# Kernel tuning notes

Measured on AMD Instinct MI355X. Metric: run time of the kernel, lower is better.

The kernel has to match this reference:

```python
import jax, jax.numpy as jnp
import numpy as np

B, T, NT = 2, 2048, 512
DIM, DEPTH, MEL, TDIM = 768, 8, 100, 512
D_INNER, NS, PH, Q = 1536, 128, 64, 64
NH = D_INNER // PH
CONV_DIM = D_INNER + 2 * NS
D_INPROJ = 2 * D_INNER + 2 * NS + NH
KCONV = 4
FFI = 2 * DIM
VOCAB = 257


def _ln(x, eps=1e-6):
    m = jnp.mean(x, -1, keepdims=True)
    v = jnp.mean((x - m) ** 2, -1, keepdims=True)
    return (x - m) * jax.lax.rsqrt(v + eps)


def _mish(x):
    return x * jnp.tanh(jax.nn.softplus(x))


def _dwconv_causal(x, w, b):
    # x: [B,T,C], w: [C,K]  depthwise causal conv (left-pad K-1)
    K = w.shape[1]
    xp = jnp.pad(x, ((0, 0), (K - 1, 0), (0, 0)))
    y = sum(xp[:, k:k + x.shape[1]] * w[:, k] for k in range(K))
    return y + b


def _ssd(xh, Bm, Cm, dt, A):
    # chunked selective-scan (Mamba SSD form). xh [B,T,H,P]; Bm,Cm [B,T,N]; dt [B,T,H]; A [H]
    Bsz, Tt, H, P = xh.shape
    N = Bm.shape[-1]
    Cn = Tt // Q
    xb = (dt[..., None] * xh).reshape(Bsz, Cn, Q, H, P)
    a = (dt * A).reshape(Bsz, Cn, Q, H)
    Bc = Bm.reshape(Bsz, Cn, Q, N)
    Cc = Cm.reshape(Bsz, Cn, Q, N)
    acum = jnp.cumsum(a, axis=2)  # [b,c,q,h]
    # intra-chunk: decay matrix exp(acum_q - acum_s) for s <= q
    Ldec = jnp.exp(acum[:, :, :, None, :] - acum[:, :, None, :, :])  # [b,c,q,s,h]
    mask = jnp.tril(jnp.ones((Q, Q), dtype=bool))
    Ldec = jnp.where(mask[None, None, :, :, None], Ldec, 0.0)
    CB = jnp.einsum('bcqn,bcsn->bcqs', Cc, Bc)
    y_in = jnp.einsum('bcqs,bcqsh,bcshp->bcqhp', CB, Ldec, xb)
    # chunk end-states
    dst = jnp.exp(acum[:, :, -1:, :] - acum)  # [b,c,q,h]
    S = jnp.einsum('bcqh,bcqn,bcqhp->bchpn', dst, Bc, xb)
    atot = jnp.exp(acum[:, :, -1, :])  # [b,c,h] total chunk decay

    def step(Hc, inp):
        at_c, S_c = inp
        return at_c[:, :, None, None] * Hc + S_c, Hc

    H0 = jnp.zeros((Bsz, H, P, N), xh.dtype)
    _, prev = jax.lax.scan(step, H0, (jnp.moveaxis(atot, 1, 0), jnp.moveaxis(S, 1, 0)))
    prev = jnp.moveaxis(prev, 0, 1)  # state entering each chunk [b,c,h,p,n]
    y_out = jnp.einsum('bcqn,bchpn->bcqhp', Cc, prev) * jnp.exp(acum)[..., None]
    return (y_in + y_out).reshape(Bsz, Tt, H, P)


def _forward(x, cond, time, text, text_table, inp_w, inp_b, pos_w1, pos_b1, pos_w2, pos_b2, t_w1, t_b1, t_w2, t_b2, adaln_w, adaln_b, in_w, conv_w, conv_b, dt_bias, A_log, Dp, rms_w, out_w, ff_w1, ff_b1, ff_w2, ff_b2, fin_w, fin_b, proj_w, proj_b):
    # timestep embedding (sinusoidal, scale 1000, freq dim 256 -> MLP)
    half = 128
    freqs = jnp.exp(-jnp.log(10000.0) / (half - 1) * jnp.arange(half, dtype=x.dtype))
    ang = 1000.0 * time[:, None] * freqs[None]
    te = jnp.concatenate([jnp.sin(ang), jnp.cos(ang)], -1)
    tvec = jax.nn.silu(te @ t_w1 + t_b1) @ t_w2 + t_b2  # [B,DIM]
    # text embedding (conv_layers=0 path): shift by 1, pad to seq_len, lookup
    idx = jnp.pad(text + 1, ((0, 0), (0, T - text.shape[1])))
    temb = text_table[idx]  # [B,T,TDIM]
    # input embedding + ConvPositionEmbedding (grouped conv k=31, groups=16, Mish x2)
    h = jnp.concatenate([x, cond, temb], -1) @ inp_w + inp_b  # [B,T,DIM]
    dn = ('NWC', 'WIO', 'NWC')
    p = jax.lax.conv_general_dilated(h, pos_w1, (1,), [(15, 15)], dimension_numbers=dn, feature_group_count=16) + pos_b1
    p = _mish(p)
    p = jax.lax.conv_general_dilated(p, pos_w2, (1,), [(15, 15)], dimension_numbers=dn, feature_group_count=16) + pos_b2
    h = h + _mish(p)
    st = jax.nn.silu(tvec)
    for l in range(DEPTH):
        mod = st @ adaln_w[l] + adaln_b[l]
        sh_msa, sc_msa, g_msa, sh_mlp, sc_mlp, g_mlp = jnp.split(mod, 6, -1)
        xn = _ln(h) * (1 + sc_msa[:, None]) + sh_msa[:, None]
        # Mamba-3 selective scan block
        zxbcdt = xn @ in_w[l]
        z = zxbcdt[..., :D_INNER]
        xBC = zxbcdt[..., D_INNER:D_INNER + CONV_DIM]
        dt = zxbcdt[..., D_INNER + CONV_DIM:]
        xBC = jax.nn.silu(_dwconv_causal(xBC, conv_w[l], conv_b[l]))
        xp = xBC[..., :D_INNER].reshape(B, T, NH, PH)
        Bm = xBC[..., D_INNER:D_INNER + NS]
        Cm = xBC[..., D_INNER + NS:]
        dt = jax.nn.softplus(dt + dt_bias[l])
        A = -jnp.exp(A_log[l])
        y = _ssd(xp, Bm, Cm, dt, A) + Dp[l][:, None] * xp
        y = y.reshape(B, T, D_INNER) * jax.nn.silu(z)
        y = y * jax.lax.rsqrt(jnp.mean(y * y, -1, keepdims=True) + 1e-5) * rms_w[l]
        h = h + g_msa[:, None] * (y @ out_w[l])
        # gated FFN
        xn = _ln(h) * (1 + sc_mlp[:, None]) + sh_mlp[:, None]
        ff = jax.nn.gelu(xn @ ff_w1[l] + ff_b1[l], approximate=True) @ ff_w2[l] + ff_b2[l]
        h = h + g_mlp[:, None] * ff
    fm = st @ fin_w + fin_b
    sc, sh = jnp.split(fm, 2, -1)
    h = _ln(h) * (1 + sc[:, None]) + sh[:, None]
    return h @ proj_w + proj_b


def setup_inputs() -> dict:
    key = jax.random.key(0)
    it = iter(jax.random.split(key, 40))

    def n(shape, s=0.02):
        return (s * jax.random.normal(next(it), shape)).astype(jnp.float32)

    inp = {
        'x': n((B, T, MEL), 1.0),
        'cond': n((B, T, MEL), 1.0),
        'time': jax.random.uniform(next(it), (B,), dtype=jnp.float32),
        'text_table': n((VOCAB, TDIM)),
        'inp_w': n((2 * MEL + TDIM, DIM)), 'inp_b': jnp.zeros((DIM,), jnp.float32),
        'pos_w1': n((31, DIM // 16, DIM), 0.05), 'pos_b1': jnp.zeros((DIM,), jnp.float32),
        'pos_w2': n((31, DIM // 16, DIM), 0.05), 'pos_b2': jnp.zeros((DIM,), jnp.float32),
        't_w1': n((256, DIM)), 't_b1': jnp.zeros((DIM,), jnp.float32),
        't_w2': n((DIM, DIM)), 't_b2': jnp.zeros((DIM,), jnp.float32),
        'adaln_w': n((DEPTH, DIM, 6 * DIM)), 'adaln_b': jnp.zeros((DEPTH, 6 * DIM), jnp.float32),
        'in_w': n((DEPTH, DIM, D_INPROJ)),
        'conv_w': n((DEPTH, CONV_DIM, KCONV), 0.2), 'conv_b': jnp.zeros((DEPTH, CONV_DIM), jnp.float32),
        'dt_bias': n((DEPTH, NH), 0.5),
        'A_log': jnp.log(jnp.tile(jnp.arange(1, NH + 1, dtype=jnp.float32), (DEPTH, 1))),
        'Dp': jnp.ones((DEPTH, NH), jnp.float32),
        'rms_w': jnp.ones((DEPTH, D_INNER), jnp.float32),
        'out_w': n((DEPTH, D_INNER, DIM)),
        'ff_w1': n((DEPTH, DIM, FFI)), 'ff_b1': jnp.zeros((DEPTH, FFI), jnp.float32),
        'ff_w2': n((DEPTH, FFI, DIM)), 'ff_b2': jnp.zeros((DEPTH, DIM), jnp.float32),
        'fin_w': n((DIM, 2 * DIM)), 'fin_b': jnp.zeros((2 * DIM,), jnp.float32),
        'proj_w': n((DIM, MEL)), 'proj_b': jnp.zeros((MEL,), jnp.float32),
    }
    inp['text'] = jax.random.randint(next(it), (B, NT), 0, 256)
    return inp


def reference(x, cond, time, text, text_table, inp_w, inp_b, pos_w1, pos_b1, pos_w2, pos_b2, t_w1, t_b1, t_w2, t_b2, adaln_w, adaln_b, in_w, conv_w, conv_b, dt_bias, A_log, Dp, rms_w, out_w, ff_w1, ff_b1, ff_w2, ff_b2, fin_w, fin_b, proj_w, proj_b):
    return _forward(x, cond, time, text, text_table, inp_w, inp_b, pos_w1, pos_b1, pos_w2, pos_b2, t_w1, t_b1, t_w2, t_b2, adaln_w, adaln_b, in_w, conv_w, conv_b, dt_bias, A_log, Dp, rms_w, out_w, ff_w1, ff_b1, ff_w2, ff_b2, fin_w, fin_b, proj_w, proj_b)
```

## Files before the change

### kernel.cpp

```cpp
#include <hip/hip_runtime.h>
#include <math.h>

constexpr int Bv = 2, Tv = 2048, NTv = 512;
constexpr int DIMv = 768, DEPTHv = 8, MELv = 100, TDIMv = 512;
constexpr int DINNER = 1536, NSv = 128, PHv = 64, QQv = 64;
constexpr int NHv = DINNER / PHv;
constexpr int CONVD = DINNER + 2 * NSv;
constexpr int DINP = 2 * DINNER + 2 * NSv + NHv;
constexpr int KCONVv = 4, FFIv = 2 * DIMv;
constexpr int CNv = Tv / QQv;
constexpr int PCK = 1504;
constexpr int KCAT = 768;

typedef unsigned short u16;
typedef unsigned int u32;
typedef __attribute__((ext_vector_type(8))) short short8v;
typedef __attribute__((ext_vector_type(4))) float f32x4;

__device__ __forceinline__ float siluf(float x) { return x / (1.f + expf(-x)); }
__device__ __forceinline__ float softplusf(float x) { return x > 20.f ? x : log1pf(expf(x)); }
__device__ __forceinline__ float mishf(float x) { return x * tanhf(softplusf(x)); }

__device__ __forceinline__ u16 f2bf(float v) {
    u32 u = __builtin_bit_cast(u32, v);
    u32 r = (u + 0x7fffu + ((u >> 16) & 1u)) >> 16;
    return (u16)r;
}
__device__ __forceinline__ float bf2f(u16 v) {
    u32 u = (u32)v << 16;
    return __builtin_bit_cast(float, u);
}
__device__ __forceinline__ float bf2fs(short v) { return bf2f((u16)v); }

__device__ __forceinline__ void gload16(const void* g, void* l) {
    __builtin_amdgcn_global_load_lds(
        (const __attribute__((address_space(1))) u32*)g,
        (__attribute__((address_space(3))) u32*)l, 16, 0, 0);
}

__device__ __forceinline__ float blockReduceSum(float v) {
    __shared__ float red[4];
    #pragma unroll
    for (int off = 32; off > 0; off >>= 1) v += __shfl_down(v, off, 64);
    __syncthreads();
    if ((threadIdx.x & 63) == 0) red[threadIdx.x >> 6] = v;
    __syncthreads();
    return red[0] + red[1] + red[2] + red[3];
}

template <int EPI>
__device__ __forceinline__ void gemm_epi(f32x4* acc, int nfrag, int row, int col,
        int N, int ldc, const float* bias, float* Cf, u16* Cb,
        const float* modv, int goff, int mstride) {
    if (col >= N) return;
    const float bv = (EPI == 1 || EPI == 2 || EPI == 4) ? bias[col] : 0.f;
    #pragma unroll
    for (int r = 0; r < 4; r++) {
        float v = (*acc)[r] + bv;
        if (EPI == 0) {
            Cb[(size_t)(row + r) * ldc + col] = f2bf(v);
        } else if (EPI == 2) {
            float xx = v;
            v = 0.5f * xx * (1.f + tanhf(0.7978845608028654f * (xx + 0.044715f * xx * xx * xx)));
            Cb[(size_t)(row + r) * ldc + col] = f2bf(v);
        } else if (EPI == 3 || EPI == 4) {
            const int bb = (row + r) >> 11;
            float g = modv[(size_t)bb * mstride + goff + col];
            Cf[(size_t)(row + r) * ldc + col] += g * v;
        } else {
            Cf[(size_t)(row + r) * ldc + col] = v;
        }
    }
}

template <int EPI>
__global__ __launch_bounds__(256) void gemm_bf16(const u16* __restrict__ A,
        const u16* __restrict__ BT, const float* __restrict__ bias,
        float* __restrict__ Cf, u16* __restrict__ Cb,
        int M, int N, int K, int ldc,
        const float* __restrict__ modv, int goff, int mstride) {
    __shared__ __align__(16) u16 As[2][128 * 32];
    __shared__ __align__(16) u16 Bs[2][128 * 32];
    const int tid = threadIdx.x;
    const int gx = gridDim.x;
    const int nwg = gx * gridDim.y;
    int flat = blockIdx.y * gx + blockIdx.x;
    const int qq = nwg >> 3;
    flat = (flat & 7) * qq + (flat >> 3);
    const int m0 = (flat / gx) * 128, n0 = (flat % gx) * 128;
    const int lane = tid & 63;
    const int wid = tid >> 6;
    const int wm = (wid >> 1) * 64, wn = (wid & 1) * 64;
    f32x4 acc[4][4] = {};
    const int srow = tid >> 2, sseg = (tid & 3) * 8;
    const u16* Ag = A + (size_t)(m0 + srow) * K + sseg;
    const u16* Bg = BT + (size_t)(n0 + srow) * K + sseg;
    const int lr = lane & 15, lk = (lane >> 4) * 8;
    gload16(Ag, &As[0][tid * 8]);
    gload16(Ag + (size_t)64 * K, &As[0][tid * 8 + 64 * 32]);
    gload16(Bg, &Bs[0][tid * 8]);
    gload16(Bg + (size_t)64 * K, &Bs[0][tid * 8 + 64 * 32]);
    __syncthreads();
    int cur = 0;
    for (int k0 = 0; k0 < K; k0 += 32) {
        if (k0 + 32 < K) {
            const int nb = cur ^ 1, kn = k0 + 32;
            gload16(Ag + kn, &As[nb][tid * 8]);
            gload16(Ag + kn + (size_t)64 * K, &As[nb][tid * 8 + 64 * 32]);
            gload16(Bg + kn, &Bs[nb][tid * 8]);
            gload16(Bg + kn + (size_t)64 * K, &Bs[nb][tid * 8 + 64 * 32]);
        }
        short8v a_f[4], b_f[4];
        #pragma unroll
        for (int i = 0; i < 4; i++)
            a_f[i] = *(const short8v*)&As[cur][(wm + i * 16 + lr) * 32 + lk];
        #pragma unroll
        for (int j = 0; j < 4; j++)
            b_f[j] = *(const short8v*)&Bs[cur][(wn + j * 16 + lr) * 32 + lk];
        #pragma unroll
        for (int i = 0; i < 4; i++)
            #pragma unroll
            for (int j = 0; j < 4; j++)
                acc[i][j] = __builtin_amdgcn_mfma_f32_16x16x32_bf16(a_f[i], b_f[j], acc[i][j], 0, 0, 0);
        __syncthreads();
        cur ^= 1;
    }
    const int r0 = (lane >> 4) * 4;
    #pragma unroll
    for (int i = 0; i < 4; i++)
        #pragma unroll
        for (int j = 0; j < 4; j++)
            gemm_epi<EPI>(&acc[i][j], 1, m0 + wm + i * 16 + r0, n0 + wn + j * 16 + lr,
                          N, ldc, bias, Cf, Cb, modv, goff, mstride);
}

template <int EPI>
__global__ __launch_bounds__(256) void gemm_bf16s(const u16* __restrict__ A,
        const u16* __restrict__ BT, const float* __restrict__ bias,
        float* __restrict__ Cf, u16* __restrict__ Cb,
        int M, int N, int K, int ldc,
        const float* __restrict__ modv, int goff, int mstride) {
    __shared__ __align__(16) u16 As[4][64 * 32];
    __shared__ __align__(16) u16 Bs[4][128 * 32];
    const int tid = threadIdx.x;
    const int gx = gridDim.x;
    const int nwg = gx * gridDim.y;
    int flat = blockIdx.y * gx + blockIdx.x;
    const int qq = nwg >> 3;
    flat = (flat & 7) * qq + (flat >> 3);
    const int m0 = (flat / gx) * 64, n0 = (flat % gx) * 128;
    const int lane = tid & 63;
    const int wid = tid >> 6;
    const int wn = wid * 32;
    f32x4 acc[4][2] = {};
    const int srow = tid >> 2, sseg = (tid & 3) * 8;
    const u16* Ag = A + (size_t)(m0 + srow) * K + sseg;
    const u16* Bg = BT + (size_t)(n0 + srow) * K + sseg;
    const int lr = lane & 15, lk = (lane >> 4) * 8;
    auto STAGE = [&](int buf, int kk) {
        gload16(Ag + kk, &As[buf][tid * 8]);
        gload16(Bg + kk, &Bs[buf][tid * 8]);
        gload16(Bg + kk + (size_t)64 * K, &Bs[buf][tid * 8 + 64 * 32]);
    };
    auto COMP = [&](int buf) {
        short8v a_f[4], b_f[2];
        #pragma unroll
        for (int i = 0; i < 4; i++)
            a_f[i] = *(const short8v*)&As[buf][(i * 16 + lr) * 32 + lk];
        #pragma unroll
        for (int j = 0; j < 2; j++)
            b_f[j] = *(const short8v*)&Bs[buf][(wn + j * 16 + lr) * 32 + lk];
        #pragma unroll
        for (int i = 0; i < 4; i++)
            #pragma unroll
            for (int j = 0; j < 2; j++)
                acc[i][j] = __builtin_amdgcn_mfma_f32_16x16x32_bf16(a_f[i], b_f[j], acc[i][j], 0, 0, 0);
    };
    STAGE(0, 0);
    STAGE(1, 32);
    __syncthreads();
    int cur = 0;
    for (int k0 = 0; k0 < K; k0 += 64) {
        if (k0 + 64 < K) {
            STAGE((cur + 2) & 3, k0 + 64);
            STAGE((cur + 3) & 3, k0 + 96);
        }
        COMP(cur);
        COMP((cur + 1) & 3);
        __syncthreads();
        cur = (cur + 2) & 3;
    }
    const int r0 = (lane >> 4) * 4;
    #pragma unroll
    for (int i = 0; i < 4; i++)
        #pragma unroll
        for (int j = 0; j < 2; j++)
            gemm_epi<EPI>(&acc[i][j], 1, m0 + i * 16 + r0, n0 + wn + j * 16 + lr,
                          N, ldc, bias, Cf, Cb, modv, goff, mstride);
}

__global__ __launch_bounds__(256) void wt_convert_b(const float* __restrict__ W,
        u16* __restrict__ WT, int Kd, int N, int Kmax, int Npad) {
    const float* Wl = W + (size_t)blockIdx.z * Kmax * N;
    u16* WTl = WT + (size_t)blockIdx.z * Npad * Kd;
    __shared__ float t[32][33];
    const int n0 = blockIdx.x * 32, k0 = blockIdx.y * 32;
    const int c = threadIdx.x & 31, rq = (threadIdx.x >> 5) * 4;
    #pragma unroll
    for (int i = 0; i < 4; i++) {
        int n = n0 + c, k = k0 + rq + i;
        t[rq + i][c] = (n < N && k < Kmax) ? Wl[(size_t)k * N + n] : 0.f;
    }
    __syncthreads();
    #pragma unroll
    for (int i = 0; i < 4; i++)
        WTl[(size_t)(n0 + rq + i) * Kd + k0 + c] = f2bf(t[c][rq + i]);
}

__global__ __launch_bounds__(256) void pw_convert(const float* __restrict__ w,
        u16* __restrict__ WT) {
    __shared__ float t[32][33];
    const int kk0 = blockIdx.x * 32, o0 = blockIdx.y * 32;
    const int c = threadIdx.x & 31, rq = (threadIdx.x >> 5) * 4;
    #pragma unroll
    for (int i = 0; i < 4; i++) {
        int kk = kk0 + rq + i;
        t[rq + i][c] = (kk < 1488) ? w[(size_t)kk * DIMv + o0 + c] : 0.f;
    }
    __syncthreads();
    #pragma unroll
    for (int i = 0; i < 4; i++)
        WT[(size_t)(o0 + rq + i) * PCK + kk0 + c] = f2bf(t[c][rq + i]);
}

template <int IN_BF, int FUSE>
__global__ __launch_bounds__(256) void posconv_mfma(const void* __restrict__ inv,
        const u16* __restrict__ WT, const float* __restrict__ bias,
        void* __restrict__ outv) {
    __shared__ __align__(16) u16 xs[95 * 48];
    const int t0 = blockIdx.x * 64, g = blockIdx.y, b = blockIdx.z;
    const int tid = threadIdx.x;
    for (int e = tid; e < 95 * 48; e += 256) {
        int rr = e / 48, cc = e % 48;
        int t = t0 - 15 + rr;
        float v = 0.f;
        if (t >= 0 && t < Tv) {
            size_t gi = ((size_t)b * Tv + t) * DIMv + g * 48 + cc;
            v = IN_BF ? bf2f(((const u16*)inv)[gi]) : ((const float*)inv)[gi];
        }
        xs[e] = f2bf(v);
    }
    __syncthreads();
    const int lane = tid & 63, w = tid >> 6;
    const int lr = lane & 15, lq8 = (lane >> 4) * 8, rq = (lane >> 4) * 4;
    const u16* arow = &xs[(w * 16 + lr) * 48 + lq8];
    const u16* brow = &WT[(size_t)(g * 48 + lr) * PCK + lq8];
    f32x4 acc[3] = {};
    #pragma unroll 2
    for (int ks = 0; ks < PCK / 32; ks++) {
        short8v a = *(const short8v*)(arow + ks * 32);
        #pragma unroll
        for (int j = 0; j < 3; j++) {
            short8v bf = *(const short8v*)(brow + (size_t)j * 16 * PCK + ks * 32);
            acc[j] = __builtin_amdgcn_mfma_f32_16x16x32_bf16(a, bf, acc[j], 0, 0, 0);
        }
    }
    #pragma unroll
    for (int j = 0; j < 3; j++) {
        const int o = g * 48 + j * 16 + lr;
        const float bvv = bias[o];
        #pragma unroll
        for (int r = 0; r < 4; r++) {
            const int t = t0 + w * 16 + rq + r;
            float v = acc[j][r] + bvv;
            size_t gi = ((size_t)b * Tv + t) * DIMv + o;
            if (FUSE == 0) ((u16*)outv)[gi] = f2bf(mishf(v));
            else ((float*)outv)[gi] += mishf(v);
        }
    }
}

__global__ __launch_bounds__(256) void temb1_kernel(const float* __restrict__ timev,
        const float* __restrict__ t_w1, const float* __restrict__ t_b1,
        float* __restrict__ hid) {
    const int b = blockIdx.y;
    const int o = blockIdx.x * 64 + (threadIdx.x & 63);
    const int ks = threadIdx.x >> 6;
    __shared__ float te[256];
    __shared__ float part[4][64];
    {
        int j = threadIdx.x, f = j & 127;
        float fr = expf(-logf(10000.f) / 127.f * (float)f);
        float ang = 1000.f * timev[b] * fr;
        te[j] = (j < 128) ? sinf(ang) : cosf(ang);
    }
    __syncthreads();
    float acc = 0.f;
    #pragma unroll 8
    for (int k = ks * 64; k < ks * 64 + 64; k++) acc += te[k] * t_w1[(size_t)k * DIMv + o];
    part[ks][threadIdx.x & 63] = acc;
    __syncthreads();
    if (threadIdx.x < 64) {
        float r = part[0][threadIdx.x] + part[1][threadIdx.x] + part[2][threadIdx.x] + part[3][threadIdx.x]
                + t_b1[o];
        hid[b * DIMv + o] = siluf(r);
    }
}

__global__ __launch_bounds__(256) void temb2_kernel(const float* __restrict__ hid,
        const float* __restrict__ t_w2, const float* __restrict__ t_b2,
        float* __restrict__ st_out) {
    const int b = blockIdx.y;
    const int o = blockIdx.x * 64 + (threadIdx.x & 63);
    const int ks = threadIdx.x >> 6;
    __shared__ float hv[DIMv];
    __shared__ float part[4][64];
    for (int j = threadIdx.x; j < DIMv; j += 256) hv[j] = hid[b * DIMv + j];
    __syncthreads();
    float acc = 0.f;
    #pragma unroll 8
    for (int k = ks * 192; k < ks * 192 + 192; k++) acc += hv[k] * t_w2[(size_t)k * DIMv + o];
    part[ks][threadIdx.x & 63] = acc;
    __syncthreads();
    if (threadIdx.x < 64) {
        float r = part[0][threadIdx.x] + part[1][threadIdx.x] + part[2][threadIdx.x] + part[3][threadIdx.x]
                + t_b2[o];
        st_out[b * DIMv + o] = siluf(r);
    }
}

__global__ __launch_bounds__(256) void modvec_kernel(const float* __restrict__ st,
        const float* __restrict__ W, const float* __restrict__ bias,
        float* __restrict__ out, int N) {
    const int l = blockIdx.z, b = blockIdx.y;
    const int o = blockIdx.x * 64 + (threadIdx.x & 63);
    const int ks = threadIdx.x >> 6;
    __shared__ float sv[DIMv];
    __shared__ float part[4][64];
    for (int j = threadIdx.x; j < DIMv; j += 256) sv[j] = st[b * DIMv + j];
    __syncthreads();
    const float* Wl = W + (size_t)l * DIMv * N + o;
    float acc = 0.f;
    #pragma unroll 8
    for (int k = ks * 192; k < ks * 192 + 192; k++) acc += sv[k] * Wl[(size_t)k * N];
    part[ks][threadIdx.x & 63] = acc;
    __syncthreads();
    if (threadIdx.x < 64) {
        float r = part[0][threadIdx.x] + part[1][threadIdx.x] + part[2][threadIdx.x] + part[3][threadIdx.x]
                + bias[(size_t)l * N + o];
        out[((size_t)l * Bv + b) * N + o] = r;
    }
}

__global__ void concat_bf16(const float* __restrict__ x, const float* __restrict__ cond,
                            const float* __restrict__ table, const int* __restrict__ text,
                            u16* __restrict__ cat) {
    size_t i = (size_t)blockIdx.x * 256 + threadIdx.x;
    const size_t total = (size_t)Bv * Tv * KCAT;
    if (i >= total) return;
    int j = (int)(i % KCAT);
    size_t row = i / KCAT;
    int t = (int)(row % Tv), b = (int)(row / Tv);
    float v = 0.f;
    if (j < MELv) v = x[row * MELv + j];
    else if (j < 2 * MELv) v = cond[row * MELv + (j - MELv)];
    else if (j < 712) {
        int idx = (t < NTv) ? (text[b * NTv + t] + 1) : 0;
        v = table[(size_t)idx * TDIMv + (j - 2 * MELv)];
    }
    cat[i] = f2bf(v);
}

template <int BF>
__global__ __launch_bounds__(256) void ln_mod_kernel(const float* __restrict__ h,
        void* __restrict__ outv, const float* __restrict__ modv,
        int sc_off, int sh_off, int mod_stride) {
    const int row = blockIdx.x;
    const int b = row / Tv;
    const float* hr = h + (size_t)row * DIMv;
    float s = 0.f;
    for (int j = threadIdx.x; j < DIMv; j += 256) s += hr[j];
    s = blockReduceSum(s);
    const float m = s / DIMv;
    float v = 0.f;
    for (int j = threadIdx.x; j < DIMv; j += 256) { float d = hr[j] - m; v += d * d; }
    v = blockReduceSum(v);
    const float rstd = rsqrtf(v / DIMv + 1e-6f);
    const float* mb = modv + (size_t)b * mod_stride;
    for (int j = threadIdx.x; j < DIMv; j += 256) {
        float val = (hr[j] - m) * rstd * (1.f + mb[sc_off + j]) + mb[sh_off + j];
        if (BF) ((u16*)outv)[(size_t)row * DIMv + j] = f2bf(val);
        else ((float*)outv)[(size_t)row * DIMv + j] = val;
    }
}

__global__ __launch_bounds__(256) void dwconvT(const u16* __restrict__ zxb,
        const float* __restrict__ cw, const float* __restrict__ cb,
        u16* __restrict__ xT) {
    __shared__ __align__(16) u16 in_s[67 * 72];
    const int pb = blockIdx.x;
    const int c = blockIdx.y, b = blockIdx.z;
    const int bc = b * CNv + c;
    const int tid = threadIdx.x;
    for (int e = tid; e < 67 * 8; e += 256) {
        int sp = e >> 3, p8 = (e & 7) * 8;
        int t = c * 64 + sp - 3;
        short8v v = {};
        if (t >= 0)
            v = *(const short8v*)&zxb[((size_t)b * Tv + t) * DINP + DINNER + pb * 64 + p8];
        *(short8v*)&in_s[sp * 72 + p8] = v;
    }
    __syncthreads();
    const int p = tid >> 2, sb = (tid & 3) * 16;
    const int ch = pb * 64 + p;
    const float w0 = cw[ch * 4], w1 = cw[ch * 4 + 1], w2 = cw[ch * 4 + 2], w3 = cw[ch * 4 + 3];
    const float bb = cb[ch];
    short8v o0, o1;
    #pragma unroll
    for (int i = 0; i < 16; i++) {
        int s = sb + i;
        float acc = bb + bf2f(in_s[s * 72 + p]) * w0 + bf2f(in_s[(s + 1) * 72 + p]) * w1
                  + bf2f(in_s[(s + 2) * 72 + p]) * w2 + bf2f(in_s[(s + 3) * 72 + p]) * w3;
        short r = (short)f2bf(siluf(acc));
        if (i < 8) o0[i] = r; else o1[i - 8] = r;
    }
    u16* dst = xT + ((size_t)bc * DINNER + ch) * 64 + sb;
    *(short8v*)dst = o0;
    *(short8v*)(dst + 8) = o1;
}

__global__ __launch_bounds__(256) void ssd_cb(const u16* __restrict__ zxb,
        const float* __restrict__ cw, const float* __restrict__ cbv,
        u16* __restrict__ xbcBC, float* __restrict__ CBg, u16* __restrict__ BTg) {
    constexpr int ST = 136;
    __shared__ __align__(16) u16 Cs[64 * ST];
    __shared__ __align__(16) u16 Bs[64 * ST];
    const int c = blockIdx.x, b = blockIdx.y;
    const int bc = b * CNv + c;
    const int tid = threadIdx.x;
    const size_t rowbase = (size_t)b * Tv + (size_t)c * QQv;
    for (int e = tid; e < 64 * 32; e += 256) {
        int r = e >> 5, n8 = (e & 31) * 8;
        size_t row = rowbase + r;
        int t = c * 64 + r;
        const u16* base = zxb + row * DINP + DINNER + n8;
        float acc[8];
        #pragma unroll
        for (int u = 0; u < 8; u++) acc[u] = cbv[DINNER + n8 + u];
        #pragma unroll
        for (int k = 0; k < KCONVv; k++) {
            const int d = k - 3;
            if (t + d < 0) continue;
            short8v tv = *(const short8v*)(base + (ptrdiff_t)d * DINP);
            #pragma unroll
            for (int u = 0; u < 8; u++)
                acc[u] += bf2fs(tv[u]) * cw[(DINNER + n8 + u) * KCONVv + k];
        }
        short8v o;
        #pragma unroll
        for (int u = 0; u < 8; u++) o[u] = (short)f2bf(siluf(acc[u]));
        if (n8 < NSv) *(short8v*)&Bs[r * ST + n8] = o;
        else *(short8v*)&Cs[r * ST + (n8 - NSv)] = o;
        *(short8v*)&xbcBC[row * 256 + n8] = o;
    }
    __syncthreads();
    u16* btg = BTg + (size_t)bc * (NSv * QQv);
    for (int e = tid; e < 128 * 64; e += 256) {
        int n = e >> 6, s = e & 63;
        btg[e] = Bs[s * ST + n];
    }
    const int lane = tid & 63, w = tid >> 6;
    const int lr = lane & 15, lk8 = (lane >> 4) * 8, rq = (lane >> 4) * 4;
    f32x4 acc[4] = {};
    #pragma unroll
    for (int ks = 0; ks < 4; ks++) {
        short8v a = *(const short8v*)&Cs[(w * 16 + lr) * ST + ks * 32 + lk8];
        #pragma unroll
        for (int j = 0; j < 4; j++) {
            short8v bf = *(const short8v*)&Bs[(j * 16 + lr) * ST + ks * 32 + lk8];
            acc[j] = __builtin_amdgcn_mfma_f32_16x16x32_bf16(a, bf, acc[j], 0, 0, 0);
        }
    }
    float* out = CBg + (size_t)bc * 4096;
    #pragma unroll
    for (int j = 0; j < 4; j++)
        #pragma unroll
        for (int r = 0; r < 4; r++)
            out[(w * 16 + rq + r) * 64 + j * 16 + lr] = acc[j][r];
}

__global__ __launch_bounds__(256) void ssd_part1m(const u16* __restrict__ xT,
        const u16* __restrict__ BTg, const u16* __restrict__ zxb,
        const float* __restrict__ dt_bias, const float* __restrict__ A_log,
        const float* __restrict__ CBg, u16* __restrict__ ybuf,
        u16* __restrict__ Sg, float* __restrict__ acg, float* __restrict__ atg) {
    constexpr int ST64 = 72;
    __shared__ __align__(16) u16 xTs[64 * ST64];
    __shared__ __align__(16) u16 Wsm[64 * ST64];
    __shared__ __align__(16) u16 BTs[128 * ST64];
    __shared__ float ac[64], dts[64], dtrev[64];
    const int h = blockIdx.x, c = blockIdx.y, b = blockIdx.z;
    const int bc = b * CNv + c;
    const int tid = threadIdx.x;
    const size_t rowbase = (size_t)b * Tv + (size_t)c * QQv;
    const size_t bch = ((size_t)bc) * NHv + h;
    if (tid < 64) {
        float raw = bf2f(zxb[(rowbase + tid) * DINP + DINNER + CONVD + h]) + dt_bias[h];
        float dtv = softplusf(raw);
        dts[tid] = dtv;
        float v = dtv * (-expf(A_log[h]));
        #pragma unroll
        for (int off = 1; off < 64; off <<= 1) {
            float t = __shfl_up(v, off, 64);
            if (tid >= off) v += t;
        }
        ac[tid] = v;
        float v63 = __shfl(v, 63, 64);
        dtrev[tid] = dtv * expf(v63 - v);
        acg[bch * 64 + tid] = v;
        if (tid == 63) atg[bch] = expf(v63);
    }
    {
        const u16* src = xT + ((size_t)bc * DINNER + h * PHv) * 64;
        for (int e = tid; e < 64 * 8; e += 256) {
            int p = e >> 3, s8 = (e & 7) * 8;
            *(short8v*)&xTs[p * ST64 + s8] = *(const short8v*)(src + p * 64 + s8);
        }
    }
    __syncthreads();
    {
        const u16* btg = BTg + (size_t)bc * (NSv * QQv);
        for (int e = tid; e < 128 * 8; e += 256) {
            int n = e >> 3, s8 = (e & 7) * 8;
            short8v v = *(const short8v*)(btg + n * 64 + s8);
            short8v o;
            #pragma unroll
            for (int u = 0; u < 8; u++)
                o[u] = (short)f2bf(bf2fs(v[u]) * dtrev[s8 + u]);
            *(short8v*)&BTs[n * ST64 + s8] = o;
        }
        const float* cbrow = CBg + (size_t)bc * 4096;
        for (int e = tid; e < 1024; e += 256) {
            int q = e >> 4, s4 = (e & 15) * 4;
            f32x4 cb4 = *(const f32x4*)&cbrow[q * 64 + s4];
            float aq = ac[q];
            #pragma unroll
            for (int u = 0; u < 4; u++) {
                int s = s4 + u;
                float wv = (s <= q) ? cb4[u] * expf(aq - ac[s]) * dts[s] : 0.f;
                Wsm[q * ST64 + s] = f2bf(wv);
            }
        }
    }
    __syncthreads();
    const int lane = tid & 63, w = tid >> 6;
    const int lr = lane & 15, lk8 = (lane >> 4) * 8, rq = (lane >> 4) * 4;
    {
        f32x4 acc[4] = {};
        #pragma unroll
        for (int ks = 0; ks < 2; ks++) {
            short8v bf = *(const short8v*)&xTs[(w * 16 + lr) * ST64 + ks * 32 + lk8];
            #pragma unroll
            for (int i = 0; i < 4; i++) {
                short8v a = *(const short8v*)&Wsm[(i * 16 + lr) * ST64 + ks * 32 + lk8];
                acc[i] = __builtin_amdgcn_mfma_f32_16x16x32_bf16(a, bf, acc[i], 0, 0, 0);
            }
        }
        #pragma unroll
        for (int i = 0; i < 4; i++)
            #pragma unroll
            for (int r = 0; r < 4; r++) {
                int q = i * 16 + rq + r, p = w * 16 + lr;
                ybuf[(rowbase + q) * DINNER + h * PHv + p] = f2bf(acc[i][r]);
            }
    }
    {
        f32x4 acc[4][2] = {};
        #pragma unroll
        for (int ks = 0; ks < 2; ks++) {
            short8v a[4];
            #pragma unroll
            for (int i = 0; i < 4; i++)
                a[i] = *(const short8v*)&xTs[(i * 16 + lr) * ST64 + ks * 32 + lk8];
            #pragma unroll
            for (int j = 0; j < 2; j++) {
                short8v bf = *(const short8v*)&BTs[(w * 32 + j * 16 + lr) * ST64 + ks * 32 + lk8];
                #pragma unroll
                for (int i = 0; i < 4; i++)
                    acc[i][j] = __builtin_amdgcn_mfma_f32_16x16x32_bf16(a[i], bf, acc[i][j], 0, 0, 0);
            }
        }
        u16* So = Sg + bch * (PHv * NSv);
        #pragma unroll
        for (int i = 0; i < 4; i++)
            #pragma unroll
            for (int j = 0; j < 2; j++)
                #pragma unroll
                for (int r = 0; r < 4; r++)
                    So[(i * 16 + rq + r) * NSv + w * 32 + j * 16 + lr] = f2bf(acc[i][j][r]);
    }
}

__global__ void ssd_scan(u16* __restrict__ Sg, const float* __restrict__ atg) {
    int idx = blockIdx.x * 256 + threadIdx.x;
    if (idx >= Bv * NHv * PHv * NSv) return;
    int n = idx % NSv;
    int p = (idx / NSv) % PHv;
    int h = (idx / (NSv * PHv)) % NHv;
    int b = idx / (NSv * PHv * NHv);
    float H = 0.f;
    for (int c = 0; c < CNv; c++) {
        size_t bch = ((size_t)b * CNv + c) * NHv + h;
        size_t off = bch * PHv * NSv + (size_t)p * NSv + n;
        float s = bf2f(Sg[off]);
        float at = atg[bch];
        Sg[off] = f2bf(H);
        H = at * H + s;
    }
}

__global__ __launch_bounds__(256) void ssd_part2m(const u16* __restrict__ xbcBC,
        const u16* __restrict__ xT, const u16* __restrict__ Sg,
        const float* __restrict__ acg, const float* __restrict__ Dp,
        u16* __restrict__ ybuf) {
    constexpr int ST = 136;
    __shared__ __align__(16) u16 Cs[64 * ST];
    __shared__ __align__(16) u16 Ps[64 * ST];
    __shared__ float eac[64];
    const int h = blockIdx.x, c = blockIdx.y, b = blockIdx.z;
    const int bc = b * CNv + c;
    const int tid = threadIdx.x;
    const size_t rowbase = (size_t)b * Tv + (size_t)c * QQv;
    const size_t bch = ((size_t)bc) * NHv + h;
    if (tid < 64) eac[tid] = expf(acg[bch * 64 + tid]);
    for (int e = tid; e < 64 * 16; e += 256) {
        int r = e >> 4, n8 = (e & 15) * 8;
        *(short8v*)&Cs[r * ST + n8] =
            *(const short8v*)&xbcBC[(rowbase + r) * 256 + NSv + n8];
        *(short8v*)&Ps[r * ST + n8] =
            *(const short8v*)&Sg[bch * (PHv * NSv) + (size_t)r * NSv + n8];
    }
    __syncthreads();
    const int lane = tid & 63, w = tid >> 6;
    const int lr = lane & 15, lk8 = (lane >> 4) * 8, rq = (lane >> 4) * 4;
    f32x4 acc[4] = {};
    #pragma unroll
    for (int ks = 0; ks < 4; ks++) {
        short8v bf = *(const short8v*)&Ps[(w * 16 + lr) * ST + ks * 32 + lk8];
        #pragma unroll
        for (int i = 0; i < 4; i++) {
            short8v a = *(const short8v*)&Cs[(i * 16 + lr) * ST + ks * 32 + lk8];
            acc[i] = __builtin_amdgcn_mfma_f32_16x16x32_bf16(a, bf, acc[i], 0, 0, 0);
        }
    }
    const float Dh = Dp[h];
    const int p = w * 16 + lr;
    const u16* xrow = xT + ((size_t)bc * DINNER + h * PHv + p) * 64;
    #pragma unroll
    for (int i = 0; i < 4; i++)
        #pragma unroll
        for (int r = 0; r < 4; r++) {
            int q = i * 16 + rq + r;
            size_t yi = (rowbase + q) * DINNER + h * PHv + p;
            float xv = bf2f(xrow[q]);
            ybuf[yi] = f2bf(bf2f(ybuf[yi]) + acc[i][r] * eac[q] + Dh * xv);
        }
}

__global__ __launch_bounds__(256) void gate_rms_kernel(const u16* __restrict__ y,
        const u16* __restrict__ zxb, const float* __restrict__ rms_w,
        u16* __restrict__ yb) {
    const int row = blockIdx.x;
    const u16* yr = y + (size_t)row * DINNER;
    const u16* zr = zxb + (size_t)row * DINP;
    float vals[8];
    float ss = 0.f;
    const int tid = threadIdx.x;
    if (tid < 192) {
        short8v yv = *(const short8v*)(yr + tid * 8);
        short8v zv = *(const short8v*)(zr + tid * 8);
        #pragma unroll
        for (int u = 0; u < 8; u++) {
            float v = bf2fs(yv[u]) * siluf(bf2fs(zv[u]));
            vals[u] = v;
            ss += v * v;
        }
    }
    ss = blockReduceSum(ss);
    const float scale = rsqrtf(ss / DINNER + 1e-5f);
    if (tid < 192) {
        short8v outv;
        #pragma unroll
        for (int u = 0; u < 8; u++)
            outv[u] = (short)f2bf(vals[u] * scale * rms_w[tid * 8 + u]);
        *(short8v*)(yb + (size_t)row * DINNER + tid * 8) = outv;
    }
}

extern "C" void kernel_launch(void* const* d_in, const int* in_sizes, int n_in,
                              void* d_out, int out_size, void* d_ws, size_t ws_size,
                              hipStream_t stream) {
    int s3 = (in_sizes[3] == Bv * NTv) ? 1 : 0;
    const float* x      = (const float*)d_in[0];
    const float* cond   = (const float*)d_in[1];
    const float* timev  = (const float*)d_in[2];
    const int*   text   = (const int*)(s3 ? d_in[3] : d_in[32]);
    const float* table  = (const float*)d_in[3 + s3];
    const float* inp_w  = (const float*)d_in[4 + s3];
    const float* inp_b  = (const float*)d_in[5 + s3];
    const float* pos_w1 = (const float*)d_in[6 + s3];
    const float* pos_b1 = (const float*)d_in[7 + s3];
    const float* pos_w2 = (const float*)d_in[8 + s3];
    const float* pos_b2 = (const float*)d_in[9 + s3];
    const float* t_w1   = (const float*)d_in[10 + s3];
    const float* t_b1   = (const float*)d_in[11 + s3];
    const float* t_w2   = (const float*)d_in[12 + s3];
    const float* t_b2   = (const float*)d_in[13 + s3];
    const float* adaln_w= (const float*)d_in[14 + s3];
    const float* adaln_b= (const float*)d_in[15 + s3];
    const float* in_w   = (const float*)d_in[16 + s3];
    const float* conv_w = (const float*)d_in[17 + s3];
    const float* conv_b = (const float*)d_in[18 + s3];
    const float* dt_bias= (const float*)d_in[19 + s3];
    const float* A_log  = (const float*)d_in[20 + s3];
    const float* Dp     = (const float*)d_in[21 + s3];
    const float* rms_w  = (const float*)d_in[22 + s3];
    const float* out_w  = (const float*)d_in[23 + s3];
    const float* ff_w1  = (const float*)d_in[24 + s3];
    const float* ff_b1  = (const float*)d_in[25 + s3];
    const float* ff_w2  = (const float*)d_in[26 + s3];
    const float* ff_b2  = (const float*)d_in[27 + s3];
    const float* fin_w  = (const float*)d_in[28 + s3];
    const float* fin_b  = (const float*)d_in[29 + s3];
    const float* proj_w = (const float*)d_in[30 + s3];
    const float* proj_b = (const float*)d_in[31 + s3];

    float* ws = (float*)d_ws;
    const size_t n_h = (size_t)Bv * Tv * DIMv;
    size_t off = 0;
    auto nx = [&](size_t n) { float* p = ws + off; off += n; return p; };
    float* h_   = nx(n_h);
    float* ac_  = nx((size_t)Bv * CNv * NHv * QQv);
    float* at_  = nx((size_t)Bv * CNv * NHv);
    float* CB_  = nx((size_t)Bv * CNv * QQv * QQv);
    float* st_  = nx((size_t)Bv * DIMv);
    float* hid_ = nx((size_t)Bv * DIMv);
    float* mod_ = nx((size_t)DEPTHv * Bv * 6 * DIMv);
    float* fm_  = nx((size_t)Bv * 2 * DIMv);
    off = (off + 15) & ~(size_t)15;
    u16* wtin_  = (u16*)(ws + off);
    u16* wtout_ = wtin_  + (size_t)DEPTHv * 3456 * 768;
    u16* wtff1_ = wtout_ + (size_t)DEPTHv * 768 * 1536;
    u16* wtff2_ = wtff1_ + (size_t)DEPTHv * 1536 * 768;
    u16* wtinp_ = wtff2_ + (size_t)DEPTHv * 768 * 1536;
    u16* wtprj_ = wtinp_ + (size_t)768 * KCAT;
    u16* pwt1_  = wtprj_ + (size_t)128 * 768;
    u16* pwt2_  = pwt1_  + (size_t)768 * PCK;
    u16* zxb_   = pwt2_  + (size_t)768 * PCK;
    u16* xbcBC_ = zxb_   + (size_t)4096 * DINP;
    u16* xT_    = xbcBC_ + (size_t)4096 * 256;
    u16* BTg_   = xT_    + (size_t)64 * DINNER * 64;
    u16* S_     = BTg_   + (size_t)64 * NSv * 64;
    u16* yb_    = S_     + (size_t)Bv * CNv * NHv * PHv * NSv;
    u16* xnb_   = yb_    + (size_t)4096 * 1536;
    u16* actb_  = xnb_   + (size_t)4096 * 768;
    u16* xnb2_  = actb_  + (size_t)4096 * 1536;
    u16* catb_  = xnb2_  + (size_t)4096 * 768;

    const int MT = Bv * Tv;

    wt_convert_b<<<dim3(3456 / 32, 768 / 32, DEPTHv), 256, 0, stream>>>(
        in_w, wtin_, 768, DINP, DIMv, 3456);
    wt_convert_b<<<dim3(768 / 32, 1536 / 32, DEPTHv), 256, 0, stream>>>(
        out_w, wtout_, 1536, DIMv, DINNER, 768);
    wt_convert_b<<<dim3(1536 / 32, 768 / 32, DEPTHv), 256, 0, stream>>>(
        ff_w1, wtff1_, 768, FFIv, DIMv, 1536);
    wt_convert_b<<<dim3(768 / 32, 1536 / 32, DEPTHv), 256, 0, stream>>>(
        ff_w2, wtff2_, 1536, DIMv, FFIv, 768);
    wt_convert_b<<<dim3(768 / 32, KCAT / 32, 1), 256, 0, stream>>>(
        inp_w, wtinp_, KCAT, DIMv, 712, 768);
    wt_convert_b<<<dim3(128 / 32, 768 / 32, 1), 256, 0, stream>>>(
        proj_w, wtprj_, 768, MELv, DIMv, 128);
    pw_convert<<<dim3(PCK / 32, DIMv / 32), 256, 0, stream>>>(pos_w1, pwt1_);
    pw_convert<<<dim3(PCK / 32, DIMv / 32), 256, 0, stream>>>(pos_w2, pwt2_);

    temb1_kernel<<<dim3(DIMv / 64, Bv), 256, 0, stream>>>(timev, t_w1, t_b1, hid_);
    temb2_kernel<<<dim3(DIMv / 64, Bv), 256, 0, stream>>>(hid_, t_w2, t_b2, st_);
    modvec_kernel<<<dim3(6 * DIMv / 64, Bv, DEPTHv), 256, 0, stream>>>(st_, adaln_w, adaln_b, mod_, 6 * DIMv);
    modvec_kernel<<<dim3(2 * DIMv / 64, Bv, 1), 256, 0, stream>>>(st_, fin_w, fin_b, fm_, 2 * DIMv);

    concat_bf16<<<(unsigned)(((size_t)Bv * Tv * KCAT + 255) / 256), 256, 0, stream>>>(
        x, cond, table, text, catb_);
    gemm_bf16s<1><<<dim3(6, 64), 256, 0, stream>>>(
        catb_, wtinp_, inp_b, h_, nullptr, MT, DIMv, KCAT, DIMv, nullptr, 0, 0);

    posconv_mfma<0, 0><<<dim3(Tv / 64, 16, Bv), 256, 0, stream>>>(h_, pwt1_, pos_b1, xnb2_);
    posconv_mfma<1, 1><<<dim3(Tv / 64, 16, Bv), 256, 0, stream>>>(xnb2_, pwt2_, pos_b2, h_);

    for (int l = 0; l < DEPTHv; l++) {
        const float* modl = mod_ + (size_t)l * Bv * 6 * DIMv;
        const float* cwl = conv_w + (size_t)l * CONVD * KCONVv;
        const float* cbl = conv_b + (size_t)l * CONVD;
        ln_mod_kernel<1><<<MT, 256, 0, stream>>>(h_, xnb_, modl, DIMv, 0, 6 * DIMv);
        gemm_bf16<0><<<dim3(27, 32), 256, 0, stream>>>(
            xnb_, wtin_ + (size_t)l * 3456 * 768, nullptr, nullptr, zxb_,
            MT, DINP, DIMv, DINP, nullptr, 0, 0);
        dwconvT<<<dim3(DINNER / 64, CNv, Bv), 256, 0, stream>>>(zxb_, cwl, cbl, xT_);
        ssd_cb<<<dim3(CNv, Bv), 256, 0, stream>>>(zxb_, cwl, cbl, xbcBC_, CB_, BTg_);
        ssd_part1m<<<dim3(NHv, CNv, Bv), 256, 0, stream>>>(
            xT_, BTg_, zxb_, dt_bias + l * NHv, A_log + l * NHv, CB_, yb_, S_, ac_, at_);
        ssd_scan<<<(Bv * NHv * PHv * NSv + 255) / 256, 256, 0, stream>>>(S_, at_);
        ssd_part2m<<<dim3(NHv, CNv, Bv), 256, 0, stream>>>(
            xbcBC_, xT_, S_, ac_, Dp + l * NHv, yb_);
        gate_rms_kernel<<<MT, 256, 0, stream>>>(yb_, zxb_, rms_w + (size_t)l * DINNER, actb_);
        gemm_bf16s<3><<<dim3(6, 64), 256, 0, stream>>>(
            actb_, wtout_ + (size_t)l * 768 * 1536, nullptr, h_, nullptr,
            MT, DIMv, DINNER, DIMv, modl, 2 * DIMv, 6 * DIMv);
        ln_mod_kernel<1><<<MT, 256, 0, stream>>>(h_, xnb_, modl, 4 * DIMv, 3 * DIMv, 6 * DIMv);
        gemm_bf16<2><<<dim3(12, 32), 256, 0, stream>>>(
            xnb_, wtff1_ + (size_t)l * 1536 * 768, ff_b1 + (size_t)l * FFIv, nullptr, actb_,
            MT, FFIv, DIMv, FFIv, nullptr, 0, 0);
        gemm_bf16s<4><<<dim3(6, 64), 256, 0, stream>>>(
            actb_, wtff2_ + (size_t)l * 768 * 1536, ff_b2 + (size_t)l * DIMv, h_, nullptr,
            MT, DIMv, FFIv, DIMv, modl, 5 * DIMv, 6 * DIMv);
    }

    ln_mod_kernel<1><<<MT, 256, 0, stream>>>(h_, xnb_, fm_, 0, DIMv, 2 * DIMv);
    gemm_bf16s<1><<<dim3(1, 64), 256, 0, stream>>>(
        xnb_, wtprj_, proj_b, (float*)d_out, nullptr, MT, MELv, DIMv, MELv, nullptr, 0, 0);
}
```

Baseline: 2.495 ms.

## Merge depthwise conv and CB kernels into one launch; simplify skinny GEMM buffering

The dwconvT and ssd_cb kernels become a single ssd_front kernel. Blocks with selector below 24 run the x-channel depthwise conv, and the 25th block per chunk computes the B/C conv plus the CB matmul. This removes one launch per layer and lets both kinds of work run concurrently. Separately, the skinny gemm_bf16s goes from a 4-stage, two-k-step-per-iteration pipeline to plain double buffering with one 32-wide k step per iteration. That cuts LDS use, which may raise occupancy, but adds a barrier for every k step.

New measurement: 2.604 ms. 4.4% more time.

```diff
diff --git a/kernel.cpp b/kernel.cpp
--- a/kernel.cpp
+++ b/kernel.cpp
@@ -49,7 +49,7 @@
 }
 
 template <int EPI>
-__device__ __forceinline__ void gemm_epi(f32x4* acc, int nfrag, int row, int col,
+__device__ __forceinline__ void gemm_epi(f32x4* acc, int row, int col,
         int N, int ldc, const float* bias, float* Cf, u16* Cb,
         const float* modv, int goff, int mstride) {
     if (col >= N) return;
@@ -130,7 +130,7 @@
     for (int i = 0; i < 4; i++)
         #pragma unroll
         for (int j = 0; j < 4; j++)
-            gemm_epi<EPI>(&acc[i][j], 1, m0 + wm + i * 16 + r0, n0 + wn + j * 16 + lr,
+            gemm_epi<EPI>(&acc[i][j], m0 + wm + i * 16 + r0, n0 + wn + j * 16 + lr,
                           N, ldc, bias, Cf, Cb, modv, goff, mstride);
 }
 
@@ -140,8 +140,8 @@
         float* __restrict__ Cf, u16* __restrict__ Cb,
         int M, int N, int K, int ldc,
         const float* __restrict__ modv, int goff, int mstride) {
-    __shared__ __align__(16) u16 As[4][64 * 32];
-    __shared__ __align__(16) u16 Bs[4][128 * 32];
+    __shared__ __align__(16) u16 As[2][64 * 32];
+    __shared__ __align__(16) u16 Bs[2][128 * 32];
     const int tid = threadIdx.x;
     const int gx = gridDim.x;
     const int nwg = gx * gridDim.y;
@@ -157,45 +157,39 @@
     const u16* Ag = A + (size_t)(m0 + srow) * K + sseg;
     const u16* Bg = BT + (size_t)(n0 + srow) * K + sseg;
     const int lr = lane & 15, lk = (lane >> 4) * 8;
-    auto STAGE = [&](int buf, int kk) {
-        gload16(Ag + kk, &As[buf][tid * 8]);
-        gload16(Bg + kk, &Bs[buf][tid * 8]);
-        gload16(Bg + kk + (size_t)64 * K, &Bs[buf][tid * 8 + 64 * 32]);
-    };
-    auto COMP = [&](int buf) {
+    gload16(Ag, &As[0][tid * 8]);
+    gload16(Bg, &Bs[0][tid * 8]);
+    gload16(Bg + (size_t)64 * K, &Bs[0][tid * 8 + 64 * 32]);
+    __syncthreads();
+    int cur = 0;
+    for (int k0 = 0; k0 < K; k0 += 32) {
+        if (k0 + 32 < K) {
+            const int nb = cur ^ 1, kn = k0 + 32;
+            gload16(Ag + kn, &As[nb][tid * 8]);
+            gload16(Bg + kn, &Bs[nb][tid * 8]);
+            gload16(Bg + kn + (size_t)64 * K, &Bs[nb][tid * 8 + 64 * 32]);
+        }
         short8v a_f[4], b_f[2];
         #pragma unroll
         for (int i = 0; i < 4; i++)
-            a_f[i] = *(const short8v*)&As[buf][(i * 16 + lr) * 32 + lk];
+            a_f[i] = *(const short8v*)&As[cur][(i * 16 + lr) * 32 + lk];
         #pragma unroll
         for (int j = 0; j < 2; j++)
-            b_f[j] = *(const short8v*)&Bs[buf][(wn + j * 16 + lr) * 32 + lk];
+            b_f[j] = *(const short8v*)&Bs[cur][(wn + j * 16 + lr) * 32 + lk];
         #pragma unroll
         for (int i = 0; i < 4; i++)
             #pragma unroll
             for (int j = 0; j < 2; j++)
                 acc[i][j] = __builtin_amdgcn_mfma_f32_16x16x32_bf16(a_f[i], b_f[j], acc[i][j], 0, 0, 0);
-    };
-    STAGE(0, 0);
-    STAGE(1, 32);
-    __syncthreads();
-    int cur = 0;
-    for (int k0 = 0; k0 < K; k0 += 64) {
-        if (k0 + 64 < K) {
-            STAGE((cur + 2) & 3, k0 + 64);
-            STAGE((cur + 3) & 3, k0 + 96);
-        }
-        COMP(cur);
-        COMP((cur + 1) & 3);
         __syncthreads();
-        cur = (cur + 2) & 3;
+        cur ^= 1;
     }
     const int r0 = (lane >> 4) * 4;
     #pragma unroll
     for (int i = 0; i < 4; i++)
         #pragma unroll
         for (int j = 0; j < 2; j++)
-            gemm_epi<EPI>(&acc[i][j], 1, m0 + i * 16 + r0, n0 + wn + j * 16 + lr,
+            gemm_epi<EPI>(&acc[i][j], m0 + i * 16 + r0, n0 + wn + j * 16 + lr,
                           N, ldc, bias, Cf, Cb, modv, goff, mstride);
 }
 
@@ -394,99 +388,97 @@
     }
 }
 
-__global__ __launch_bounds__(256) void dwconvT(const u16* __restrict__ zxb,
-        const float* __restrict__ cw, const float* __restrict__ cb,
-        u16* __restrict__ xT) {
-    __shared__ __align__(16) u16 in_s[67 * 72];
-    const int pb = blockIdx.x;
+__global__ __launch_bounds__(256) void ssd_front(const u16* __restrict__ zxb,
+        const float* __restrict__ cw, const float* __restrict__ cbv,
+        u16* __restrict__ xT, u16* __restrict__ xbcBC,
+        float* __restrict__ CBg, u16* __restrict__ BTg) {
+    constexpr int ST = 136;
+    __shared__ __align__(16) u16 smem[64 * ST * 2];
+    const int sel = blockIdx.x;
     const int c = blockIdx.y, b = blockIdx.z;
     const int bc = b * CNv + c;
     const int tid = threadIdx.x;
-    for (int e = tid; e < 67 * 8; e += 256) {
-        int sp = e >> 3, p8 = (e & 7) * 8;
-        int t = c * 64 + sp - 3;
-        short8v v = {};
-        if (t >= 0)
-            v = *(const short8v*)&zxb[((size_t)b * Tv + t) * DINP + DINNER + pb * 64 + p8];
-        *(short8v*)&in_s[sp * 72 + p8] = v;
-    }
-    __syncthreads();
-    const int p = tid >> 2, sb = (tid & 3) * 16;
-    const int ch = pb * 64 + p;
-    const float w0 = cw[ch * 4], w1 = cw[ch * 4 + 1], w2 = cw[ch * 4 + 2], w3 = cw[ch * 4 + 3];
-    const float bb = cb[ch];
-    short8v o0, o1;
-    #pragma unroll
-    for (int i = 0; i < 16; i++) {
-        int s = sb + i;
-        float acc = bb + bf2f(in_s[s * 72 + p]) * w0 + bf2f(in_s[(s + 1) * 72 + p]) * w1
-                  + bf2f(in_s[(s + 2) * 72 + p]) * w2 + bf2f(in_s[(s + 3) * 72 + p]) * w3;
-        short r = (short)f2bf(siluf(acc));
-        if (i < 8) o0[i] = r; else o1[i - 8] = r;
-    }
-    u16* dst = xT + ((size_t)bc * DINNER + ch) * 64 + sb;
-    *(short8v*)dst = o0;
-    *(short8v*)(dst + 8) = o1;
-}
-
-__global__ __launch_bounds__(256) void ssd_cb(const u16* __restrict__ zxb,
-        const float* __restrict__ cw, const float* __restrict__ cbv,
-        u16* __restrict__ xbcBC, float* __restrict__ CBg, u16* __restrict__ BTg) {
-    constexpr int ST = 136;
-    __shared__ __align__(16) u16 Cs[64 * ST];
-    __shared__ __align__(16) u16 Bs[64 * ST];
-    const int c = blockIdx.x, b = blockIdx.y;
-    const int bc = b * CNv + c;
-    const int tid = threadIdx.x;
     const size_t rowbase = (size_t)b * Tv + (size_t)c * QQv;
-    for (int e = tid; e < 64 * 32; e += 256) {
-        int r = e >> 5, n8 = (e & 31) * 8;
-        size_t row = rowbase + r;
-        int t = c * 64 + r;
-        const u16* base = zxb + row * DINP + DINNER + n8;
-        float acc[8];
-        #pragma unroll
-        for (int u = 0; u < 8; u++) acc[u] = cbv[DINNER + n8 + u];
-        #pragma unroll
-        for (int k = 0; k < KCONVv; k++) {
-            const int d = k - 3;
-            if (t + d < 0) continue;
-            short8v tv = *(const short8v*)(base + (ptrdiff_t)d * DINP);
-            #pragma unroll
-            for (int u = 0; u < 8; u++)
-                acc[u] += bf2fs(tv[u]) * cw[(DINNER + n8 + u) * KCONVv + k];
-        }
-        short8v o;
-        #pragma unroll
-        for (int u = 0; u < 8; u++) o[u] = (short)f2bf(siluf(acc[u]));
-        if (n8 < NSv) *(short8v*)&Bs[r * ST + n8] = o;
-        else *(short8v*)&Cs[r * ST + (n8 - NSv)] = o;
-        *(short8v*)&xbcBC[row * 256 + n8] = o;
-    }
-    __syncthreads();
-    u16* btg = BTg + (size_t)bc * (NSv * QQv);
-    for (int e = tid; e < 128 * 64; e += 256) {
-        int n = e >> 6, s = e & 63;
-        btg[e] = Bs[s * ST + n];
-    }
-    const int lane = tid & 63, w = tid >> 6;
-    const int lr = lane & 15, lk8 = (lane >> 4) * 8, rq = (lane >> 4) * 4;
-    f32x4 acc[4] = {};
-    #pragma unroll
-    for (int ks = 0; ks < 4; ks++) {
-        short8v a = *(const short8v*)&Cs[(w * 16 + lr) * ST + ks * 32 + lk8];
-        #pragma unroll
-        for (int j = 0; j < 4; j++) {
-            short8v bf = *(const short8v*)&Bs[(j * 16 + lr) * ST + ks * 32 + lk8];
-            acc[j] = __builtin_amdgcn_mfma_f32_16x16x32_bf16(a, bf, acc[j], 0, 0, 0);
-        }
-    }
-    float* out = CBg + (size_t)bc * 4096;
-    #pragma unroll
-    for (int j = 0; j < 4; j++)
-        #pragma unroll
-        for (int r = 0; r < 4; r++)
-            out[(w * 16 + rq + r) * 64 + j * 16 + lr] = acc[j][r];
+    if (sel < 24) {
+        u16* in_s = smem;
+        const int pb = sel;
+        for (int e = tid; e < 67 * 8; e += 256) {
+            int sp = e >> 3, p8 = (e & 7) * 8;
+            int t = c * 64 + sp - 3;
+            short8v v = {};
+            if (t >= 0)
+                v = *(const short8v*)&zxb[((size_t)b * Tv + t) * DINP + DINNER + pb * 64 + p8];
+            *(short8v*)&in_s[sp * 72 + p8] = v;
+        }
+        __syncthreads();
+        const int p = tid >> 2, sb = (tid & 3) * 16;
+        const int ch = pb * 64 + p;
+        const float w0 = cw[ch * 4], w1 = cw[ch * 4 + 1], w2 = cw[ch * 4 + 2], w3 = cw[ch * 4 + 3];
+        const float bb = cbv[ch];
+        short8v o0, o1;
+        #pragma unroll
+        for (int i = 0; i < 16; i++) {
+            int s = sb + i;
+            float acc = bb + bf2f(in_s[s * 72 + p]) * w0 + bf2f(in_s[(s + 1) * 72 + p]) * w1
+                      + bf2f(in_s[(s + 2) * 72 + p]) * w2 + bf2f(in_s[(s + 3) * 72 + p]) * w3;
+            short r = (short)f2bf(siluf(acc));
+            if (i < 8) o0[i] = r; else o1[i - 8] = r;
+        }
+        u16* dst = xT + ((size_t)bc * DINNER + ch) * 64 + sb;
+        *(short8v*)dst = o0;
+        *(short8v*)(dst + 8) = o1;
+    } else {
+        u16* Cs = smem;
+        u16* Bs = smem + 64 * ST;
+        for (int e = tid; e < 64 * 32; e += 256) {
+            int r = e >> 5, n8 = (e & 31) * 8;
+            size_t row = rowbase + r;
+            int t = c * 64 + r;
+            const u16* base = zxb + row * DINP + DINNER + n8;
+            float acc[8];
+            #pragma unroll
+            for (int u = 0; u < 8; u++) acc[u] = cbv[DINNER + n8 + u];
+            #pragma unroll
+            for (int k = 0; k < KCONVv; k++) {
+                const int d = k - 3;
+                if (t + d < 0) continue;
+                short8v tv = *(const short8v*)(base + (ptrdiff_t)d * DINP);
+                #pragma unroll
+                for (int u = 0; u < 8; u++)
+                    acc[u] += bf2fs(tv[u]) * cw[(DINNER + n8 + u) * KCONVv + k];
+            }
+            short8v o;
+            #pragma unroll
+            for (int u = 0; u < 8; u++) o[u] = (short)f2bf(siluf(acc[u]));
+            if (n8 < NSv) *(short8v*)&Bs[r * ST + n8] = o;
+            else *(short8v*)&Cs[r * ST + (n8 - NSv)] = o;
+            *(short8v*)&xbcBC[row * 256 + n8] = o;
+        }
+        __syncthreads();
+        u16* btg = BTg + (size_t)bc * (NSv * QQv);
+        for (int e = tid; e < 128 * 64; e += 256) {
+            int n = e >> 6, s = e & 63;
+            btg[e] = Bs[s * ST + n];
+        }
+        const int lane = tid & 63, w = tid >> 6;
+        const int lr = lane & 15, lk8 = (lane >> 4) * 8, rq = (lane >> 4) * 4;
+        f32x4 acc[4] = {};
+        #pragma unroll
+        for (int ks = 0; ks < 4; ks++) {
+            short8v a = *(const short8v*)&Cs[(w * 16 + lr) * ST + ks * 32 + lk8];
+            #pragma unroll
+            for (int j = 0; j < 4; j++) {
+                short8v bf = *(const short8v*)&Bs[(j * 16 + lr) * ST + ks * 32 + lk8];
+                acc[j] = __builtin_amdgcn_mfma_f32_16x16x32_bf16(a, bf, acc[j], 0, 0, 0);
+            }
+        }
+        float* out = CBg + (size_t)bc * 4096;
+        #pragma unroll
+        for (int j = 0; j < 4; j++)
+            #pragma unroll
+            for (int r = 0; r < 4; r++)
+                out[(w * 16 + rq + r) * 64 + j * 16 + lr] = acc[j][r];
+    }
 }
 
 __global__ __launch_bounds__(256) void ssd_part1m(const u16* __restrict__ xT,
@@ -805,8 +797,8 @@
         gemm_bf16<0><<<dim3(27, 32), 256, 0, stream>>>(
             xnb_, wtin_ + (size_t)l * 3456 * 768, nullptr, nullptr, zxb_,
             MT, DINP, DIMv, DINP, nullptr, 0, 0);
-        dwconvT<<<dim3(DINNER / 64, CNv, Bv), 256, 0, stream>>>(zxb_, cwl, cbl, xT_);
-        ssd_cb<<<dim3(CNv, Bv), 256, 0, stream>>>(zxb_, cwl, cbl, xbcBC_, CB_, BTg_);
+        ssd_front<<<dim3(25, CNv, Bv), 256, 0, stream>>>(
+            zxb_, cwl, cbl, xT_, xbcBC_, CB_, BTg_);
         ssd_part1m<<<dim3(NHv, CNv, Bv), 256, 0, stream>>>(
             xT_, BTg_, zxb_, dt_bias + l * NHv, A_log + l * NHv, CB_, yb_, S_, ac_, at_);
         ssd_scan<<<(Bv * NHv * PHv * NSv + 255) / 256, 256, 0, stream>>>(S_, at_);
```
